# Kernel optimization log

Hardware: AMD Instinct MI355X
Metric: run time of the kernel (lower is better)

Reference implementation:

```python
import jax, jax.numpy as jnp
import numpy as np

E = 8          # num_experts
TOP_K = 2      # router top-k
ALPHA = 1.702  # swigluoai alpha
LIMIT = 7.0    # swigluoai clamp limit


def setup_inputs() -> dict:
    key = jax.random.key(0)
    ks = jax.random.split(key, 7)
    B, S, H, I = 2, 1024, 1024, 1024
    s = 1.0 / np.sqrt(H)  # keep activations O(1), realistic init scale
    return {
        "x": jax.random.normal(ks[0], (B, S, H), jnp.float32),
        "router_weight": jax.random.normal(ks[1], (E, H), jnp.float32) * s,
        "router_bias": jax.random.normal(ks[2], (E,), jnp.float32) * 0.01,
        "w1": jax.random.normal(ks[3], (E, H, 2 * I), jnp.float32) * s,  # interleaved gate/up
        "w1_bias": jax.random.normal(ks[4], (E, 2 * I), jnp.float32) * 0.01,
        "w2": jax.random.normal(ks[5], (E, I, H), jnp.float32) * s,
        "w2_bias": jax.random.normal(ks[6], (E, H), jnp.float32) * 0.01,
    }


def _moe(x, router_weight, router_bias, w1, w1_bias, w2, w2_bias):
    B, S, H = x.shape
    xf = x.reshape(-1, H)                                   # [T, H]
    # ---- router: softmax over expert logits, then top-k ----
    logits = xf @ router_weight.T + router_bias             # [T, E]
    probs = jax.nn.softmax(logits, axis=-1)
    expert_weights, expert_ids = jax.lax.top_k(probs, TOP_K)  # [T, k]
    # combine weights scattered to dense [T, E] (no normalization: normalize_expert_weights=None)
    combine = jnp.sum(jax.nn.one_hot(expert_ids, E, dtype=xf.dtype)
                      * expert_weights[..., None], axis=1)  # [T, E]
    # ---- grouped MLP, expressed densely per expert (reference semantics) ----
    h = jnp.einsum('th,ehi->eti', xf, w1) + w1_bias[:, None, :]   # [E, T, 2I]
    gate = h[..., 0::2]                                          # interleaved layout
    up = h[..., 1::2]
    gate = jnp.minimum(gate, LIMIT)                              # swigluoai: clamp gate max
    up = jnp.clip(up, -LIMIT, LIMIT)                             # clamp up both sides
    glu = gate * jax.nn.sigmoid(gate * ALPHA)
    act = (up + 1.0) * glu                                       # [E, T, I]
    y = jnp.einsum('eti,eih->eth', act, w2) + w2_bias[:, None, :]  # [E, T, H]
    out = jnp.einsum('eth,te->th', y, combine)                   # weighted combine
    return out.reshape(B, S, H), expert_weights


def reference(x, router_weight, router_bias, w1, w1_bias, w2, w2_bias):
    return _moe(x, router_weight, router_bias, w1, w1_bias, w2, w2_bias)
```

## Files before the change

### kernel.cpp

```cpp
#include <hip/hip_runtime.h>
#include <cstdint>
#include <cstddef>

typedef unsigned short u16;
typedef short bf16x8 __attribute__((ext_vector_type(8)));
typedef float floatx4 __attribute__((ext_vector_type(4)));

#define GLD16(gp, sp) __builtin_amdgcn_global_load_lds(                      \
    (const __attribute__((address_space(1))) void*)(gp),                     \
    (__attribute__((address_space(3))) void*)(sp), 16, 0, 0)

__device__ __forceinline__ u16 f2bf(float f) {
  unsigned u = __float_as_uint(f);
  u += 0x7fffu + ((u >> 16) & 1u);
  return (u16)(u >> 16);
}

__global__ void cvt_x_kernel(const float4* __restrict__ in, u16* __restrict__ out, int n4) {
  int i = blockIdx.x * blockDim.x + threadIdx.x;
  if (i >= n4) return;
  float4 v = in[i];
  ushort4 o;
  o.x = f2bf(v.x); o.y = f2bf(v.y); o.z = f2bf(v.z); o.w = f2bf(v.w);
  ((ushort4*)out)[i] = o;
}

__global__ void transpose_cvt_kernel(const float* __restrict__ in, u16* __restrict__ out,
                                     int R, int C) {
  __shared__ float tile[32][33];
  size_t base = (size_t)blockIdx.z * (size_t)R * (size_t)C;
  int c0 = blockIdx.x * 32, r0 = blockIdx.y * 32;
  int tx = threadIdx.x, ty = threadIdx.y;
#pragma unroll
  for (int k = 0; k < 32; k += 8)
    tile[ty + k][tx] = in[base + (size_t)(r0 + ty + k) * C + (c0 + tx)];
  __syncthreads();
#pragma unroll
  for (int k = 0; k < 32; k += 8)
    out[base + (size_t)(c0 + ty + k) * R + (r0 + tx)] = f2bf(tile[tx][ty + k]);
}

__global__ void router_kernel(const float* __restrict__ x, const float* __restrict__ rw,
                              const float* __restrict__ rb, float* __restrict__ ew,
                              int* __restrict__ eids, float* __restrict__ eprobs) {
  const int wave = threadIdx.x >> 6, lane = threadIdx.x & 63;
  const int t = blockIdx.x * 4 + wave;
  const float4* xv = (const float4*)(x + (size_t)t * 1024);
  float acc[8];
#pragma unroll
  for (int e = 0; e < 8; ++e) acc[e] = 0.f;
  for (int j = lane; j < 256; j += 64) {
    float4 xx = xv[j];
#pragma unroll
    for (int e = 0; e < 8; ++e) {
      float4 wv = ((const float4*)(rw + (size_t)e * 1024))[j];
      acc[e] += xx.x * wv.x + xx.y * wv.y + xx.z * wv.z + xx.w * wv.w;
    }
  }
#pragma unroll
  for (int e = 0; e < 8; ++e) {
    float v = acc[e];
#pragma unroll
    for (int off = 32; off > 0; off >>= 1) v += __shfl_down(v, off);
    acc[e] = v;
  }
  if (lane == 0) {
    float p[8];
    float mx = -1e30f;
#pragma unroll
    for (int e = 0; e < 8; ++e) { p[e] = acc[e] + rb[e]; mx = fmaxf(mx, p[e]); }
    float sum = 0.f;
#pragma unroll
    for (int e = 0; e < 8; ++e) { p[e] = __expf(p[e] - mx); sum += p[e]; }
    float inv = 1.f / sum;
#pragma unroll
    for (int e = 0; e < 8; ++e) p[e] *= inv;
    int i0 = 0;
#pragma unroll
    for (int e = 1; e < 8; ++e) if (p[e] > p[i0]) i0 = e;
    int i1 = (i0 == 0) ? 1 : 0;
#pragma unroll
    for (int e = 0; e < 8; ++e) if (e != i0 && e != i1 && p[e] > p[i1]) i1 = e;
    ew[t * 2 + 0] = p[i0];
    ew[t * 2 + 1] = p[i1];
    eids[t * 2 + 0] = i0;
    eids[t * 2 + 1] = i1;
    eprobs[t * 2 + 0] = p[i0];
    eprobs[t * 2 + 1] = p[i1];
  }
}

__global__ void build_lists_kernel(const int* __restrict__ eids, const float* __restrict__ eprobs,
                                   int* __restrict__ row_token, float* __restrict__ row_scale,
                                   int* __restrict__ meta) {
  __shared__ int cnt[8], base[8], cur[8];
  const int tid = threadIdx.x;
  if (tid < 8) { cnt[tid] = 0; cur[tid] = 0; }
  __syncthreads();
  for (int t = tid; t < 2048; t += 256) {
    atomicAdd(&cnt[eids[t * 2 + 0]], 1);
    atomicAdd(&cnt[eids[t * 2 + 1]], 1);
  }
  __syncthreads();
  if (tid == 0) {
    int off = 0, w = 0;
    for (int e = 0; e < 8; ++e) {
      base[e] = off;
      meta[48 + e] = off;
      int nb = (cnt[e] + 127) >> 7;
      for (int rb = 0; rb < nb; ++rb) meta[1 + w++] = (e << 8) | rb;
      off += nb << 7;
    }
    meta[0] = w;
  }
  __syncthreads();
  for (int s = tid; s < 5120; s += 256) { row_token[s] = -1; row_scale[s] = 0.f; }
  __syncthreads();
  for (int t = tid; t < 2048; t += 256) {
#pragma unroll
    for (int k = 0; k < 2; ++k) {
      int e = eids[t * 2 + k];
      int s = base[e] + atomicAdd(&cur[e], 1);
      row_token[s] = t;
      row_scale[s] = eprobs[t * 2 + k];
    }
  }
}

__global__ void bias_init_kernel(const int* __restrict__ eids, const float* __restrict__ eprobs,
                                 const float* __restrict__ w2b, float* __restrict__ out) {
  int idx = blockIdx.x * 256 + threadIdx.x;
  int t = idx >> 10, h = idx & 1023;
  int e0 = eids[t * 2], e1 = eids[t * 2 + 1];
  out[idx] = eprobs[t * 2] * w2b[e0 * 1024 + h] + eprobs[t * 2 + 1] * w2b[e1 * 1024 + h];
}

__global__ __launch_bounds__(256) void gemm1_act_kernel(
    const u16* __restrict__ xb, const u16* __restrict__ w1t,
    const float* __restrict__ w1b,
    const int* __restrict__ row_token, const float* __restrict__ row_scale,
    const int* __restrict__ meta, u16* __restrict__ actS) {
  if ((int)blockIdx.x >= meta[0]) return;
  __shared__ __align__(16) u16 As[128 * 32];
  __shared__ __align__(16) u16 Bs[128 * 32];
  const int w = meta[1 + blockIdx.x];
  const int e = w >> 8, rb = w & 255;
  const int slotB = meta[48 + e] + rb * 128;
  const int colBase = blockIdx.y * 128;
  const int tid = threadIdx.x, lane = tid & 63, wave = tid >> 6;
  const int row16 = lane & 15, chunk = lane >> 4;
  const u16* Bt = w1t + (size_t)e * 2048 * 1024;
  const u16* aP[2]; const u16* bP[2];
#pragma unroll
  for (int r = 0; r < 2; ++r) {
    int g = r * 4 + wave;
    int tk = row_token[slotB + g * 16 + row16];
    if (tk < 0) tk = 0;
    aP[r] = xb + (size_t)tk * 1024 + chunk * 8;
    bP[r] = Bt + (size_t)(colBase + g * 16 + row16) * 1024 + chunk * 8;
  }
  const int wr = wave >> 1, wc = wave & 1;
  floatx4 acc[4][4];
#pragma unroll
  for (int mi = 0; mi < 4; ++mi)
#pragma unroll
    for (int ni = 0; ni < 4; ++ni) acc[mi][ni] = floatx4{0.f, 0.f, 0.f, 0.f};

  for (int kt = 0; kt < 32; ++kt) {
    const int k = kt * 32;
    GLD16(aP[0] + k, As + wave * 512);
    GLD16(bP[0] + k, Bs + wave * 512);
    GLD16(aP[1] + k, As + (4 + wave) * 512);
    GLD16(bP[1] + k, Bs + (4 + wave) * 512);
    __syncthreads();
    bf16x8 af[4], bfr[4];
#pragma unroll
    for (int mi = 0; mi < 4; ++mi) af[mi] = *(const bf16x8*)(As + (wr * 4 + mi) * 512 + lane * 8);
#pragma unroll
    for (int ni = 0; ni < 4; ++ni) bfr[ni] = *(const bf16x8*)(Bs + (wc * 4 + ni) * 512 + lane * 8);
#pragma unroll
    for (int mi = 0; mi < 4; ++mi)
#pragma unroll
      for (int ni = 0; ni < 4; ++ni)
        acc[mi][ni] = __builtin_amdgcn_mfma_f32_16x16x32_bf16(af[mi], bfr[ni], acc[mi][ni], 0, 0, 0);
    __syncthreads();
  }

  const int cl = lane & 15, ql = lane >> 4;
#pragma unroll
  for (int mi = 0; mi < 4; ++mi) {
#pragma unroll
    for (int r = 0; r < 4; ++r) {
      const int slot = slotB + wr * 64 + mi * 16 + ql * 4 + r;
      const float c = row_scale[slot];
#pragma unroll
      for (int ni = 0; ni < 4; ++ni) {
        const int n = colBase + wc * 64 + ni * 16 + cl;
        float v = acc[mi][ni][r] + w1b[e * 2048 + n];
        float o = __shfl_xor(v, 1);
        if ((lane & 1) == 0) {
          float g = fminf(v, 7.f);
          float u = fminf(fmaxf(o, -7.f), 7.f);
          float sg = 1.f / (1.f + __expf(-1.702f * g));
          float a = (u + 1.f) * (g * sg);
          actS[(size_t)slot * 1024 + (n >> 1)] = f2bf(c * a);
        }
      }
    }
  }
}

__global__ __launch_bounds__(256) void gemm2_add_kernel(
    const u16* __restrict__ actS, const u16* __restrict__ w2t,
    const int* __restrict__ row_token, const int* __restrict__ meta,
    float* __restrict__ out) {
  if ((int)blockIdx.x >= meta[0]) return;
  __shared__ __align__(16) u16 As[128 * 32];
  __shared__ __align__(16) u16 Bs[128 * 32];
  const int w = meta[1 + blockIdx.x];
  const int e = w >> 8, rb = w & 255;
  const int slotB = meta[48 + e] + rb * 128;
  const int colBase = blockIdx.y * 128;
  const int tid = threadIdx.x, lane = tid & 63, wave = tid >> 6;
  const int row16 = lane & 15, chunk = lane >> 4;
  const u16* Bt = w2t + (size_t)e * 1024 * 1024;
  const u16* aP[2]; const u16* bP[2];
#pragma unroll
  for (int r = 0; r < 2; ++r) {
    int g = r * 4 + wave;
    aP[r] = actS + (size_t)(slotB + g * 16 + row16) * 1024 + chunk * 8;
    bP[r] = Bt + (size_t)(colBase + g * 16 + row16) * 1024 + chunk * 8;
  }
  const int wr = wave >> 1, wc = wave & 1;
  floatx4 acc[4][4];
#pragma unroll
  for (int mi = 0; mi < 4; ++mi)
#pragma unroll
    for (int ni = 0; ni < 4; ++ni) acc[mi][ni] = floatx4{0.f, 0.f, 0.f, 0.f};

  for (int kt = 0; kt < 32; ++kt) {
    const int k = kt * 32;
    GLD16(aP[0] + k, As + wave * 512);
    GLD16(bP[0] + k, Bs + wave * 512);
    GLD16(aP[1] + k, As + (4 + wave) * 512);
    GLD16(bP[1] + k, Bs + (4 + wave) * 512);
    __syncthreads();
    bf16x8 af[4], bfr[4];
#pragma unroll
    for (int mi = 0; mi < 4; ++mi) af[mi] = *(const bf16x8*)(As + (wr * 4 + mi) * 512 + lane * 8);
#pragma unroll
    for (int ni = 0; ni < 4; ++ni) bfr[ni] = *(const bf16x8*)(Bs + (wc * 4 + ni) * 512 + lane * 8);
#pragma unroll
    for (int mi = 0; mi < 4; ++mi)
#pragma unroll
      for (int ni = 0; ni < 4; ++ni)
        acc[mi][ni] = __builtin_amdgcn_mfma_f32_16x16x32_bf16(af[mi], bfr[ni], acc[mi][ni], 0, 0, 0);
    __syncthreads();
  }

  const int cl = lane & 15, ql = lane >> 4;
#pragma unroll
  for (int mi = 0; mi < 4; ++mi)
#pragma unroll
    for (int r = 0; r < 4; ++r) {
      const int slot = slotB + wr * 64 + mi * 16 + ql * 4 + r;
      const int tok = row_token[slot];
      if (tok < 0) continue;
#pragma unroll
      for (int ni = 0; ni < 4; ++ni) {
        const int col = colBase + wc * 64 + ni * 16 + cl;
        atomicAdd(out + (size_t)tok * 1024 + col, acc[mi][ni][r]);
      }
    }
}

extern "C" void kernel_launch(void* const* d_in, const int* in_sizes, int n_in,
                              void* d_out, int out_size, void* d_ws, size_t ws_size,
                              hipStream_t stream) {
  const float* x   = (const float*)d_in[0];
  const float* rw  = (const float*)d_in[1];
  const float* rb  = (const float*)d_in[2];
  const float* w1  = (const float*)d_in[3];
  const float* w1b = (const float*)d_in[4];
  const float* w2  = (const float*)d_in[5];
  const float* w2b = (const float*)d_in[6];
  float* out = (float*)d_out;
  float* ew  = out + (size_t)2048 * 1024;

  char* ws = (char*)d_ws;
  u16* xb        = (u16*)(ws);
  u16* w1t       = (u16*)(ws + (4ull << 20));
  u16* w2t       = (u16*)(ws + (36ull << 20));
  u16* actS      = (u16*)(ws + (52ull << 20));
  int* eids      = (int*)(ws + (62ull << 20));
  float* eprobs  = (float*)(ws + (62ull << 20) + (16 << 10));
  int* row_token = (int*)(ws + (62ull << 20) + (32 << 10));
  float* row_scale = (float*)(ws + (62ull << 20) + (52 << 10));
  int* meta      = (int*)(ws + (62ull << 20) + (72 << 10));

  cvt_x_kernel<<<2048, 256, 0, stream>>>((const float4*)x, xb, 2048 * 1024 / 4);
  transpose_cvt_kernel<<<dim3(64, 32, 8), dim3(32, 8), 0, stream>>>(w1, w1t, 1024, 2048);
  transpose_cvt_kernel<<<dim3(32, 32, 8), dim3(32, 8), 0, stream>>>(w2, w2t, 1024, 1024);
  router_kernel<<<512, 256, 0, stream>>>(x, rw, rb, ew, eids, eprobs);
  build_lists_kernel<<<1, 256, 0, stream>>>(eids, eprobs, row_token, row_scale, meta);
  bias_init_kernel<<<8192, 256, 0, stream>>>(eids, eprobs, w2b, out);
  gemm1_act_kernel<<<dim3(40, 16), 256, 0, stream>>>(xb, w1t, w1b, row_token, row_scale, meta, actS);
  gemm2_add_kernel<<<dim3(40, 8), 256, 0, stream>>>(actS, w2t, row_token, meta, out);
}
```

Baseline: 271.4 us.

## Fuse prep kernels, shrink GEMM N-tiles, split-K gemm2, XCD-aware block mapping

Merges the x conversion, both weight transpose-conversions and the router into one launch, with wider transpose tiles and paired bf16 stores. Both grouped GEMMs move to 128x64 tiles with a 1D grid whose column tiles are mapped so blocks sharing a weight column land on the same XCD, and gemm2 gains a 2-way split-K over its atomic accumulation. The bias init is vectorised to float4. The intent is less launch overhead, more blocks for better CU occupancy, and better L2 locality, at the cost of more A-tile reloads and twice as many atomics in gemm2.

```diff
diff --git a/kernel.cpp b/kernel.cpp
--- a/kernel.cpp
+++ b/kernel.cpp
@@ -16,77 +16,96 @@
   return (u16)(u >> 16);
 }
 
-__global__ void cvt_x_kernel(const float4* __restrict__ in, u16* __restrict__ out, int n4) {
-  int i = blockIdx.x * blockDim.x + threadIdx.x;
-  if (i >= n4) return;
-  float4 v = in[i];
-  ushort4 o;
-  o.x = f2bf(v.x); o.y = f2bf(v.y); o.z = f2bf(v.z); o.w = f2bf(v.w);
-  ((ushort4*)out)[i] = o;
-}
-
-__global__ void transpose_cvt_kernel(const float* __restrict__ in, u16* __restrict__ out,
-                                     int R, int C) {
-  __shared__ float tile[32][33];
-  size_t base = (size_t)blockIdx.z * (size_t)R * (size_t)C;
-  int c0 = blockIdx.x * 32, r0 = blockIdx.y * 32;
-  int tx = threadIdx.x, ty = threadIdx.y;
-#pragma unroll
-  for (int k = 0; k < 32; k += 8)
-    tile[ty + k][tx] = in[base + (size_t)(r0 + ty + k) * C + (c0 + tx)];
-  __syncthreads();
-#pragma unroll
-  for (int k = 0; k < 32; k += 8)
-    out[base + (size_t)(c0 + ty + k) * R + (r0 + tx)] = f2bf(tile[tx][ty + k]);
-}
-
-__global__ void router_kernel(const float* __restrict__ x, const float* __restrict__ rw,
-                              const float* __restrict__ rb, float* __restrict__ ew,
-                              int* __restrict__ eids, float* __restrict__ eprobs) {
-  const int wave = threadIdx.x >> 6, lane = threadIdx.x & 63;
-  const int t = blockIdx.x * 4 + wave;
-  const float4* xv = (const float4*)(x + (size_t)t * 1024);
-  float acc[8];
-#pragma unroll
-  for (int e = 0; e < 8; ++e) acc[e] = 0.f;
-  for (int j = lane; j < 256; j += 64) {
-    float4 xx = xv[j];
+__global__ __launch_bounds__(256) void prep_kernel(
+    const float* __restrict__ x, const float* __restrict__ rw, const float* __restrict__ rbias,
+    const float* __restrict__ w1, const float* __restrict__ w2,
+    u16* __restrict__ xb, u16* __restrict__ w1t, u16* __restrict__ w2t,
+    float* __restrict__ ew, int* __restrict__ eids, float* __restrict__ eprobs) {
+  __shared__ float lds[64 * 33];
+  const int b = blockIdx.x, tid = threadIdx.x;
+  if (b < 1024) {
+    const float4* in4 = (const float4*)x;
+    ushort4* out4 = (ushort4*)xb;
+    int i = (b << 8) + tid;
+#pragma unroll
+    for (int rep = 0; rep < 2; ++rep, i += 262144) {
+      float4 v = in4[i];
+      ushort4 o;
+      o.x = f2bf(v.x); o.y = f2bf(v.y); o.z = f2bf(v.z); o.w = f2bf(v.w);
+      out4[i] = o;
+    }
+  } else if (b < 13312) {
+    const float* in; u16* out; int C, r0, c0;
+    if (b < 9216) {
+      int b2 = b - 1024, e = b2 >> 10, rem = b2 & 1023;
+      C = 2048; r0 = (rem >> 6) << 6; c0 = (rem & 63) << 5;
+      in = w1 + (size_t)e * 2097152; out = w1t + (size_t)e * 2097152;
+    } else {
+      int b2 = b - 9216, e = b2 >> 9, rem = b2 & 511;
+      C = 1024; r0 = (rem >> 5) << 6; c0 = (rem & 31) << 5;
+      in = w2 + (size_t)e * 1048576; out = w2t + (size_t)e * 1048576;
+    }
+    const int tx = tid & 31, ty = tid >> 5;
+#pragma unroll
+    for (int k = 0; k < 8; ++k) {
+      int row = k * 8 + ty;
+      lds[row * 33 + tx] = in[(size_t)(r0 + row) * C + c0 + tx];
+    }
+    __syncthreads();
+#pragma unroll
+    for (int k = 0; k < 4; ++k) {
+      int cc = k * 8 + ty;
+      ushort2 v;
+      v.x = f2bf(lds[(tx * 2) * 33 + cc]);
+      v.y = f2bf(lds[(tx * 2 + 1) * 33 + cc]);
+      *(ushort2*)(out + (size_t)(c0 + cc) * 1024 + r0 + tx * 2) = v;
+    }
+  } else {
+    const int wave = tid >> 6, lane = tid & 63;
+    const int t = ((b - 13312) << 2) + wave;
+    const float4* xv = (const float4*)(x + (size_t)t * 1024);
+    float acc[8];
+#pragma unroll
+    for (int e = 0; e < 8; ++e) acc[e] = 0.f;
+    for (int j = lane; j < 256; j += 64) {
+      float4 xx = xv[j];
+#pragma unroll
+      for (int e = 0; e < 8; ++e) {
+        float4 wv = ((const float4*)(rw + (size_t)e * 1024))[j];
+        acc[e] += xx.x * wv.x + xx.y * wv.y + xx.z * wv.z + xx.w * wv.w;
+      }
+    }
 #pragma unroll
     for (int e = 0; e < 8; ++e) {
-      float4 wv = ((const float4*)(rw + (size_t)e * 1024))[j];
-      acc[e] += xx.x * wv.x + xx.y * wv.y + xx.z * wv.z + xx.w * wv.w;
-    }
-  }
-#pragma unroll
-  for (int e = 0; e < 8; ++e) {
-    float v = acc[e];
-#pragma unroll
-    for (int off = 32; off > 0; off >>= 1) v += __shfl_down(v, off);
-    acc[e] = v;
-  }
-  if (lane == 0) {
-    float p[8];
-    float mx = -1e30f;
-#pragma unroll
-    for (int e = 0; e < 8; ++e) { p[e] = acc[e] + rb[e]; mx = fmaxf(mx, p[e]); }
-    float sum = 0.f;
-#pragma unroll
-    for (int e = 0; e < 8; ++e) { p[e] = __expf(p[e] - mx); sum += p[e]; }
-    float inv = 1.f / sum;
-#pragma unroll
-    for (int e = 0; e < 8; ++e) p[e] *= inv;
-    int i0 = 0;
-#pragma unroll
-    for (int e = 1; e < 8; ++e) if (p[e] > p[i0]) i0 = e;
-    int i1 = (i0 == 0) ? 1 : 0;
-#pragma unroll
-    for (int e = 0; e < 8; ++e) if (e != i0 && e != i1 && p[e] > p[i1]) i1 = e;
-    ew[t * 2 + 0] = p[i0];
-    ew[t * 2 + 1] = p[i1];
-    eids[t * 2 + 0] = i0;
-    eids[t * 2 + 1] = i1;
-    eprobs[t * 2 + 0] = p[i0];
-    eprobs[t * 2 + 1] = p[i1];
+      float v = acc[e];
+#pragma unroll
+      for (int off = 32; off > 0; off >>= 1) v += __shfl_down(v, off);
+      acc[e] = v;
+    }
+    if (lane == 0) {
+      float p[8];
+      float mx = -1e30f;
+#pragma unroll
+      for (int e = 0; e < 8; ++e) { p[e] = acc[e] + rbias[e]; mx = fmaxf(mx, p[e]); }
+      float sum = 0.f;
+#pragma unroll
+      for (int e = 0; e < 8; ++e) { p[e] = __expf(p[e] - mx); sum += p[e]; }
+      float inv = 1.f / sum;
+#pragma unroll
+      for (int e = 0; e < 8; ++e) p[e] *= inv;
+      int i0 = 0;
+#pragma unroll
+      for (int e = 1; e < 8; ++e) if (p[e] > p[i0]) i0 = e;
+      int i1 = (i0 == 0) ? 1 : 0;
+#pragma unroll
+      for (int e = 0; e < 8; ++e) if (e != i0 && e != i1 && p[e] > p[i1]) i1 = e;
+      ew[t * 2 + 0] = p[i0];
+      ew[t * 2 + 1] = p[i1];
+      eids[t * 2 + 0] = i0;
+      eids[t * 2 + 1] = i1;
+      eprobs[t * 2 + 0] = p[i0];
+      eprobs[t * 2 + 1] = p[i1];
+    }
   }
 }
 
@@ -130,9 +149,17 @@
 __global__ void bias_init_kernel(const int* __restrict__ eids, const float* __restrict__ eprobs,
                                  const float* __restrict__ w2b, float* __restrict__ out) {
   int idx = blockIdx.x * 256 + threadIdx.x;
-  int t = idx >> 10, h = idx & 1023;
-  int e0 = eids[t * 2], e1 = eids[t * 2 + 1];
-  out[idx] = eprobs[t * 2] * w2b[e0 * 1024 + h] + eprobs[t * 2 + 1] * w2b[e1 * 1024 + h];
+  int t = idx >> 8, h4 = idx & 255;
+  const float4* b4 = (const float4*)w2b;
+  float4 v0 = b4[eids[2 * t] * 256 + h4];
+  float4 v1 = b4[eids[2 * t + 1] * 256 + h4];
+  float p0 = eprobs[2 * t], p1 = eprobs[2 * t + 1];
+  float4 r;
+  r.x = p0 * v0.x + p1 * v1.x;
+  r.y = p0 * v0.y + p1 * v1.y;
+  r.z = p0 * v0.z + p1 * v1.z;
+  r.w = p0 * v0.w + p1 * v1.w;
+  ((float4*)out)[idx] = r;
 }
 
 __global__ __launch_bounds__(256) void gemm1_act_kernel(
@@ -140,48 +167,46 @@
     const float* __restrict__ w1b,
     const int* __restrict__ row_token, const float* __restrict__ row_scale,
     const int* __restrict__ meta, u16* __restrict__ actS) {
-  if ((int)blockIdx.x >= meta[0]) return;
-  __shared__ __align__(16) u16 As[128 * 32];
-  __shared__ __align__(16) u16 Bs[128 * 32];
-  const int w = meta[1 + blockIdx.x];
-  const int e = w >> 8, rb = w & 255;
-  const int slotB = meta[48 + e] + rb * 128;
-  const int colBase = blockIdx.y * 128;
+  const int d = blockIdx.x;
+  const int xcd = d & 7, i = d >> 3;
+  const int work = i >> 2;
+  if (work >= meta[0]) return;
+  const int colBase = (xcd + ((i & 3) << 3)) << 6;
+  const int wk = meta[1 + work];
+  const int e = wk >> 8, rb = wk & 255;
+  const int slotB = meta[48 + e] + (rb << 7);
+  __shared__ __align__(16) u16 As[4096];
+  __shared__ __align__(16) u16 Bs[2048];
   const int tid = threadIdx.x, lane = tid & 63, wave = tid >> 6;
   const int row16 = lane & 15, chunk = lane >> 4;
-  const u16* Bt = w1t + (size_t)e * 2048 * 1024;
-  const u16* aP[2]; const u16* bP[2];
-#pragma unroll
-  for (int r = 0; r < 2; ++r) {
-    int g = r * 4 + wave;
-    int tk = row_token[slotB + g * 16 + row16];
-    if (tk < 0) tk = 0;
-    aP[r] = xb + (size_t)tk * 1024 + chunk * 8;
-    bP[r] = Bt + (size_t)(colBase + g * 16 + row16) * 1024 + chunk * 8;
-  }
+  const u16* Bt = w1t + (size_t)e * 2097152;
+  int tk0 = row_token[slotB + wave * 16 + row16];       if (tk0 < 0) tk0 = 0;
+  int tk1 = row_token[slotB + (wave + 4) * 16 + row16]; if (tk1 < 0) tk1 = 0;
+  const u16* aP0 = xb + (size_t)tk0 * 1024 + chunk * 8;
+  const u16* aP1 = xb + (size_t)tk1 * 1024 + chunk * 8;
+  const u16* bP  = Bt + (size_t)(colBase + wave * 16 + row16) * 1024 + chunk * 8;
   const int wr = wave >> 1, wc = wave & 1;
-  floatx4 acc[4][4];
+  floatx4 acc[4][2];
 #pragma unroll
   for (int mi = 0; mi < 4; ++mi)
 #pragma unroll
-    for (int ni = 0; ni < 4; ++ni) acc[mi][ni] = floatx4{0.f, 0.f, 0.f, 0.f};
+    for (int ni = 0; ni < 2; ++ni) acc[mi][ni] = floatx4{0.f, 0.f, 0.f, 0.f};
 
   for (int kt = 0; kt < 32; ++kt) {
     const int k = kt * 32;
-    GLD16(aP[0] + k, As + wave * 512);
-    GLD16(bP[0] + k, Bs + wave * 512);
-    GLD16(aP[1] + k, As + (4 + wave) * 512);
-    GLD16(bP[1] + k, Bs + (4 + wave) * 512);
-    __syncthreads();
-    bf16x8 af[4], bfr[4];
+    GLD16(aP0 + k, As + wave * 512);
+    GLD16(aP1 + k, As + (4 + wave) * 512);
+    GLD16(bP + k, Bs + wave * 512);
+    __syncthreads();
+    bf16x8 af[4], bfr[2];
 #pragma unroll
     for (int mi = 0; mi < 4; ++mi) af[mi] = *(const bf16x8*)(As + (wr * 4 + mi) * 512 + lane * 8);
 #pragma unroll
-    for (int ni = 0; ni < 4; ++ni) bfr[ni] = *(const bf16x8*)(Bs + (wc * 4 + ni) * 512 + lane * 8);
+    for (int ni = 0; ni < 2; ++ni) bfr[ni] = *(const bf16x8*)(Bs + (wc * 2 + ni) * 512 + lane * 8);
 #pragma unroll
     for (int mi = 0; mi < 4; ++mi)
 #pragma unroll
-      for (int ni = 0; ni < 4; ++ni)
+      for (int ni = 0; ni < 2; ++ni)
         acc[mi][ni] = __builtin_amdgcn_mfma_f32_16x16x32_bf16(af[mi], bfr[ni], acc[mi][ni], 0, 0, 0);
     __syncthreads();
   }
@@ -194,8 +219,8 @@
       const int slot = slotB + wr * 64 + mi * 16 + ql * 4 + r;
       const float c = row_scale[slot];
 #pragma unroll
-      for (int ni = 0; ni < 4; ++ni) {
-        const int n = colBase + wc * 64 + ni * 16 + cl;
+      for (int ni = 0; ni < 2; ++ni) {
+        const int n = colBase + wc * 32 + ni * 16 + cl;
         float v = acc[mi][ni][r] + w1b[e * 2048 + n];
         float o = __shfl_xor(v, 1);
         if ((lane & 1) == 0) {
@@ -214,46 +239,47 @@
     const u16* __restrict__ actS, const u16* __restrict__ w2t,
     const int* __restrict__ row_token, const int* __restrict__ meta,
     float* __restrict__ out) {
-  if ((int)blockIdx.x >= meta[0]) return;
-  __shared__ __align__(16) u16 As[128 * 32];
-  __shared__ __align__(16) u16 Bs[128 * 32];
-  const int w = meta[1 + blockIdx.x];
-  const int e = w >> 8, rb = w & 255;
-  const int slotB = meta[48 + e] + rb * 128;
-  const int colBase = blockIdx.y * 128;
+  const int d = blockIdx.x;
+  const int xcd = d & 7, i = d >> 3;
+  const int j = i >> 1;
+  const int ks = (j >= 40) ? 1 : 0;
+  const int work = j - ks * 40;
+  if (work >= meta[0]) return;
+  const int colBase = (xcd + ((i & 1) << 3)) << 6;
+  const int k0 = ks << 9;
+  const int wk = meta[1 + work];
+  const int e = wk >> 8, rb = wk & 255;
+  const int slotB = meta[48 + e] + (rb << 7);
+  __shared__ __align__(16) u16 As[4096];
+  __shared__ __align__(16) u16 Bs[2048];
   const int tid = threadIdx.x, lane = tid & 63, wave = tid >> 6;
   const int row16 = lane & 15, chunk = lane >> 4;
-  const u16* Bt = w2t + (size_t)e * 1024 * 1024;
-  const u16* aP[2]; const u16* bP[2];
-#pragma unroll
-  for (int r = 0; r < 2; ++r) {
-    int g = r * 4 + wave;
-    aP[r] = actS + (size_t)(slotB + g * 16 + row16) * 1024 + chunk * 8;
-    bP[r] = Bt + (size_t)(colBase + g * 16 + row16) * 1024 + chunk * 8;
-  }
+  const u16* Bt = w2t + (size_t)e * 1048576;
+  const u16* aP0 = actS + (size_t)(slotB + wave * 16 + row16) * 1024 + chunk * 8;
+  const u16* aP1 = actS + (size_t)(slotB + (wave + 4) * 16 + row16) * 1024 + chunk * 8;
+  const u16* bP  = Bt + (size_t)(colBase + wave * 16 + row16) * 1024 + chunk * 8;
   const int wr = wave >> 1, wc = wave & 1;
-  floatx4 acc[4][4];
+  floatx4 acc[4][2];
 #pragma unroll
   for (int mi = 0; mi < 4; ++mi)
 #pragma unroll
-    for (int ni = 0; ni < 4; ++ni) acc[mi][ni] = floatx4{0.f, 0.f, 0.f, 0.f};
-
-  for (int kt = 0; kt < 32; ++kt) {
-    const int k = kt * 32;
-    GLD16(aP[0] + k, As + wave * 512);
-    GLD16(bP[0] + k, Bs + wave * 512);
-    GLD16(aP[1] + k, As + (4 + wave) * 512);
-    GLD16(bP[1] + k, Bs + (4 + wave) * 512);
-    __syncthreads();
-    bf16x8 af[4], bfr[4];
+    for (int ni = 0; ni < 2; ++ni) acc[mi][ni] = floatx4{0.f, 0.f, 0.f, 0.f};
+
+  for (int kt = 0; kt < 16; ++kt) {
+    const int k = k0 + kt * 32;
+    GLD16(aP0 + k, As + wave * 512);
+    GLD16(aP1 + k, As + (4 + wave) * 512);
+    GLD16(bP + k, Bs + wave * 512);
+    __syncthreads();
+    bf16x8 af[4], bfr[2];
 #pragma unroll
     for (int mi = 0; mi < 4; ++mi) af[mi] = *(const bf16x8*)(As + (wr * 4 + mi) * 512 + lane * 8);
 #pragma unroll
-    for (int ni = 0; ni < 4; ++ni) bfr[ni] = *(const bf16x8*)(Bs + (wc * 4 + ni) * 512 + lane * 8);
+    for (int ni = 0; ni < 2; ++ni) bfr[ni] = *(const bf16x8*)(Bs + (wc * 2 + ni) * 512 + lane * 8);
 #pragma unroll
     for (int mi = 0; mi < 4; ++mi)
 #pragma unroll
-      for (int ni = 0; ni < 4; ++ni)
+      for (int ni = 0; ni < 2; ++ni)
         acc[mi][ni] = __builtin_amdgcn_mfma_f32_16x16x32_bf16(af[mi], bfr[ni], acc[mi][ni], 0, 0, 0);
     __syncthreads();
   }
@@ -267,8 +293,8 @@
       const int tok = row_token[slot];
       if (tok < 0) continue;
 #pragma unroll
-      for (int ni = 0; ni < 4; ++ni) {
-        const int col = colBase + wc * 64 + ni * 16 + cl;
+      for (int ni = 0; ni < 2; ++ni) {
+        const int col = colBase + wc * 32 + ni * 16 + cl;
         atomicAdd(out + (size_t)tok * 1024 + col, acc[mi][ni][r]);
       }
     }
@@ -298,12 +324,9 @@
   float* row_scale = (float*)(ws + (62ull << 20) + (52 << 10));
   int* meta      = (int*)(ws + (62ull << 20) + (72 << 10));
 
-  cvt_x_kernel<<<2048, 256, 0, stream>>>((const float4*)x, xb, 2048 * 1024 / 4);
-  transpose_cvt_kernel<<<dim3(64, 32, 8), dim3(32, 8), 0, stream>>>(w1, w1t, 1024, 2048);
-  transpose_cvt_kernel<<<dim3(32, 32, 8), dim3(32, 8), 0, stream>>>(w2, w2t, 1024, 1024);
-  router_kernel<<<512, 256, 0, stream>>>(x, rw, rb, ew, eids, eprobs);
+  prep_kernel<<<13824, 256, 0, stream>>>(x, rw, rb, w1, w2, xb, w1t, w2t, ew, eids, eprobs);
   build_lists_kernel<<<1, 256, 0, stream>>>(eids, eprobs, row_token, row_scale, meta);
-  bias_init_kernel<<<8192, 256, 0, stream>>>(eids, eprobs, w2b, out);
-  gemm1_act_kernel<<<dim3(40, 16), 256, 0, stream>>>(xb, w1t, w1b, row_token, row_scale, meta, actS);
-  gemm2_add_kernel<<<dim3(40, 8), 256, 0, stream>>>(actS, w2t, row_token, meta, out);
-}
+  bias_init_kernel<<<2048, 256, 0, stream>>>(eids, eprobs, w2b, out);
+  gemm1_act_kernel<<<1280, 256, 0, stream>>>(xb, w1t, w1b, row_token, row_scale, meta, actS);
+  gemm2_add_kernel<<<1280, 256, 0, stream>>>(actS, w2t, row_token, meta, out);
+}
```

After: 274.2 us. Within noise of the previous version (+1.0%).
